# Performance work log

Measured on AMD Instinct MI355X. Metric: run time of the kernel, lower is better.

## Reference

```python
import jax, jax.numpy as jnp
import numpy as np

# RON cell constants (from repo defaults)
DT = 0.01
GAMMA = 1.0
EPS = 1.0
RHO_M = 1.0

T, N_INP = 2048, 128
N_MOD, N_HID = 64, 256


def setup_inputs() -> dict:
    key = jax.random.key(0)
    k = jax.random.split(key, 7)
    x = jax.random.normal(k[0], (T, N_INP), dtype=jnp.float32)
    initial_states = jax.random.normal(k[1], (N_MOD, 2, N_HID), dtype=jnp.float32)
    # wm: Linear(n_hid, n_hid, bias=False), rescaled to spectral radius rho_m
    wm = jax.random.normal(k[2], (N_HID, N_HID), dtype=jnp.float32) / np.float32(np.sqrt(N_HID))
    spec = np.abs(np.linalg.eigvals(np.asarray(wm, dtype=np.float64))).max()
    wm_weight = (wm * np.float32(RHO_M / spec)).astype(jnp.float32)
    # binary connection matrix (stored as float Parameter in the original)
    connection_matrix = (jax.random.uniform(k[3], (N_MOD, N_MOD)) < 0.5).astype(jnp.float32)
    x2h = jax.random.normal(k[4], (N_MOD, N_HID, N_INP), dtype=jnp.float32) / np.float32(np.sqrt(N_INP))
    h2h = jax.random.normal(k[5], (N_MOD, N_HID, N_HID), dtype=jnp.float32) / np.float32(np.sqrt(N_HID))
    bias = 0.1 * jax.random.normal(k[6], (N_MOD, N_HID), dtype=jnp.float32)
    return {
        "x": x,
        "initial_states": initial_states,
        "wm_weight": wm_weight,
        "connection_matrix": connection_matrix,
        "x2h": x2h,
        "h2h": h2h,
        "bias": bias,
    }


def reference(x, initial_states, wm_weight, connection_matrix, x2h, h2h, bias):
    """Returns (states_seq, feedback_seq).
    states_seq:   (T+1, n_modules, 2, n_hid)  -- state_list stacked
    feedback_seq: (T,   n_modules, n_hid)     -- per-step feedback (input_list minus the x[0] prefix)
    """

    def step(carry, x_t):
        states, outs = carry                       # (N,2,H), (N,H)
        # feedback = connection_matrix @ wm(prev_outs)
        fb = connection_matrix @ (outs @ wm_weight.T)            # (N, H)
        hy, hz = states[:, 0], states[:, 1]                       # (N, H)
        pre = (
            jnp.einsum("nhi,i->nh", x2h, x_t)
            + jnp.einsum("nho,no->nh", h2h, hy)
            + bias
            + fb
        )
        hz_new = hz + DT * (jnp.tanh(pre) - GAMMA * hy - EPS * hz)
        hy_new = hy + DT * hz_new
        new_states = jnp.stack([hy_new, hz_new], axis=1)          # (N, 2, H)
        # outs for next step = first state (hy), as in `outs = states[:, 0]`
        return (new_states, hy_new), (new_states, fb)

    outs0 = jnp.zeros((N_MOD, N_HID), dtype=x.dtype)  # initial_outs=None path
    (_, _), (states_hist, fb_hist) = jax.lax.scan(step, (initial_states, outs0), x)
    states_seq = jnp.concatenate([initial_states[None], states_hist], axis=0)
    return states_seq, fb_hist
```

## Files before the change

### kernel.cpp

```cpp
#include <hip/hip_runtime.h>
#include <hip/hip_bf16.h>
#include <math.h>

#define T_STEPS 2048
#define N_MOD   64
#define N_HID   256
#define N_INP   128

typedef unsigned long long ull;

__device__ __forceinline__ void AG_STF(float* p, float v) {
  __hip_atomic_store(p, v, __ATOMIC_RELAXED, __HIP_MEMORY_SCOPE_AGENT);
}
__device__ __forceinline__ void AG_STU(unsigned* p, unsigned v) {
  __hip_atomic_store(p, v, __ATOMIC_RELAXED, __HIP_MEMORY_SCOPE_AGENT);
}
__device__ __forceinline__ unsigned AG_LDU(const unsigned* p) {
  return __hip_atomic_load(p, __ATOMIC_RELAXED, __HIP_MEMORY_SCOPE_AGENT);
}

__global__ __launch_bounds__(512) void init_kernel(
    const float* __restrict__ init, float* __restrict__ out_states)
{
  const int idx = blockIdx.x * 512 + threadIdx.x;
  out_states[idx] = init[idx];
}

__global__ __launch_bounds__(256, 2) void xpre_kernel(
    const float* __restrict__ x, const float* __restrict__ x2h,
    float* __restrict__ out)
{
  __shared__ float xl[64 * N_INP];
  const int tb = blockIdx.x;
  const int n  = blockIdx.y;
  const int t  = threadIdx.x;

  const float4* xs  = (const float4*)(x + (size_t)tb * 64 * N_INP);
  float4*       xld = (float4*)xl;
  for (int k = t; k < 64 * N_INP / 4; k += 256) xld[k] = xs[k];

  float w[N_INP];
  const float* wrow = x2h + ((size_t)n * N_HID + t) * N_INP;
#pragma unroll
  for (int j = 0; j < N_INP; j += 4) {
    const float4 a = *(const float4*)(wrow + j);
    w[j] = a.x; w[j+1] = a.y; w[j+2] = a.z; w[j+3] = a.w;
  }
  __syncthreads();

  for (int tt = 0; tt < 64; ++tt) {
    float a0=0.f, a1=0.f, a2=0.f, a3=0.f;
#pragma unroll
    for (int j = 0; j < N_INP; j += 4) {
      const float4 h4 = *(const float4*)&xl[tt * N_INP + j];
      a0 = fmaf(w[j],   h4.x, a0);
      a1 = fmaf(w[j+1], h4.y, a1);
      a2 = fmaf(w[j+2], h4.z, a2);
      a3 = fmaf(w[j+3], h4.w, a3);
    }
    out[((size_t)(tb*64 + tt) * N_MOD + n) * N_HID + t] = (a0+a1)+(a2+a3);
  }
}

__global__ __launch_bounds__(256) void step_kernel(
    int k, const float* __restrict__ wm, const float* __restrict__ conn,
    const float* __restrict__ h2h, const float* __restrict__ bias,
    float* __restrict__ out_states, float* __restrict__ out_fb)
{
  const int b  = blockIdx.x;
  const int m  = b >> 2;
  const int q  = b & 3;
  const int i  = threadIdx.x;
  const int ro = i & 63;
  const int jq = i >> 6;

  __shared__ float hym[N_HID];
  __shared__ float u[N_HID];
  __shared__ float redr[256];
  __shared__ float redf[256];

  const float* hyk = out_states + (size_t)k * N_MOD * 512;

  hym[i] = hyk[(size_t)m * 512 + i];
  {
    float ua=0.f, ub=0.f, uc=0.f, ud=0.f;
#pragma unroll
    for (int mm = 0; mm < N_MOD; mm += 4) {
      ua = fmaf(conn[m * N_MOD + mm + 0], hyk[(size_t)(mm + 0) * 512 + i], ua);
      ub = fmaf(conn[m * N_MOD + mm + 1], hyk[(size_t)(mm + 1) * 512 + i], ub);
      uc = fmaf(conn[m * N_MOD + mm + 2], hyk[(size_t)(mm + 2) * 512 + i], uc);
      ud = fmaf(conn[m * N_MOD + mm + 3], hyk[(size_t)(mm + 3) * 512 + i], ud);
    }
    u[i] = (ua + ub) + (uc + ud);
  }
  float xq = 0.f, hyv = 0.f, hzv = 0.f, bv = 0.f;
  if (i < 64) {
    const int hu = q * 64 + i;
    xq  = out_fb[((size_t)k * N_MOD + m) * N_HID + hu];
    hyv = hyk[(size_t)m * 512 + hu];
    hzv = hyk[(size_t)m * 512 + 256 + hu];
    bv  = bias[m * N_HID + hu];
  }
  __syncthreads();

  {
    const int h = q * 64 + ro;
    const float* hrow = h2h + ((size_t)m * N_HID + h) * N_HID + jq * 64;
    const float* wrow = wm  + (size_t)h * N_HID + jq * 64;
    float r0=0.f, r1=0.f, r2=0.f, r3=0.f;
    float f0=0.f, f1=0.f, f2=0.f, f3=0.f;
#pragma unroll
    for (int j = 0; j < 64; j += 4) {
      const float4 a  = *(const float4*)(hrow + j);
      const float4 w4 = *(const float4*)(wrow + j);
      const float4 hv = *(const float4*)(&hym[jq * 64 + j]);
      const float4 uv = *(const float4*)(&u[jq * 64 + j]);
      r0 = fmaf(a.x, hv.x, r0);  f0 = fmaf(w4.x, uv.x, f0);
      r1 = fmaf(a.y, hv.y, r1);  f1 = fmaf(w4.y, uv.y, f1);
      r2 = fmaf(a.z, hv.z, r2);  f2 = fmaf(w4.z, uv.z, f2);
      r3 = fmaf(a.w, hv.w, r3);  f3 = fmaf(w4.w, uv.w, f3);
    }
    redr[i] = (r0 + r1) + (r2 + r3);
    redf[i] = (f0 + f1) + (f2 + f3);
  }
  __syncthreads();

  if (i < 64) {
    const int hu = q * 64 + i;
    const float r  = (redr[i] + redr[i + 64]) + (redr[i + 128] + redr[i + 192]);
    const float fb = (k == 0) ? 0.f
                   : (redf[i] + redf[i + 64]) + (redf[i + 128] + redf[i + 192]);
    const float pre = xq + r + bv + fb;
    const float th  = tanhf(pre);
    const float hzn = hzv + 0.01f * (th - hyv - hzv);
    const float hyn = hyv + 0.01f * hzn;
    const size_t ob = ((size_t)(k + 1) * N_MOD + m) * 512;
    out_states[ob + hu]       = hyn;
    out_states[ob + 256 + hu] = hzn;
    out_fb[((size_t)k * N_MOD + m) * N_HID + hu] = fb;
  }
}

__global__ __launch_bounds__(256) void archnet_persist(
    const float* __restrict__ init, const float* __restrict__ wm,
    const float* __restrict__ conn, const float* __restrict__ h2h,
    const float* __restrict__ bias,
    float* __restrict__ out_states, float* __restrict__ out_fb,
    unsigned* __restrict__ flags)
{
  __shared__ float wA[64 * 256];
  __shared__ float hym_l[4 * 68];
  __shared__ float u_l[4 * 68];
  __shared__ float connrow[N_MOD];

  const int b  = blockIdx.x;
  const int m  = b >> 2;
  const int q  = b & 3;
  const int i  = threadIdx.x;
  const int r  = i >> 2;
  const int c4 = i & 3;
  const int hq = q * 64 + r;
  const int pi = (i >> 6) * 68 + (i & 63);

  if (i < N_MOD) connrow[i] = conn[m * N_MOD + i];
  u_l[pi] = 0.f;

  for (int idx = i; idx < 64 * 64; idx += 256) {
    const int rr = idx >> 6, g = idx & 63;
    const float4 a = *(const float4*)(h2h + ((size_t)m * N_HID + q * 64 + rr) * N_HID + g * 4);
    *(float4*)&wA[rr * 256 + (g ^ (rr & 7)) * 4] = a;
  }

  float hyv = 0.f, hzv = 0.f, bv = 0.f, xq = 0.f;
  if (c4 == 0) {
    hyv = init[(size_t)m * 512 + hq];
    hzv = init[(size_t)m * 512 + 256 + hq];
    bv  = bias[m * N_HID + hq];
    xq  = out_fb[(size_t)m * N_HID + hq];
  }

  const float* wrow = wm + (size_t)hq * N_HID + c4 * 64;

  for (int k = 0; k < T_STEPS; ++k) {
    if (k > 0 && i < 64) {
      const unsigned kk = (unsigned)k;
      for (;;) {
        const unsigned f0 = AG_LDU(&flags[i * 4 + 0]);
        const unsigned f1 = AG_LDU(&flags[i * 4 + 1]);
        const unsigned f2 = AG_LDU(&flags[i * 4 + 2]);
        const unsigned f3 = AG_LDU(&flags[i * 4 + 3]);
        if (!__any(f0 < kk || f1 < kk || f2 < kk || f3 < kk)) break;
        __builtin_amdgcn_s_sleep(1);
      }
    }
    __syncthreads();

    const float* hyk = out_states + (size_t)k * (N_MOD * 512);
    hym_l[pi] = hyk[(size_t)m * 512 + i];
    if (k > 0) {
      float ua=0.f, ub=0.f, uc=0.f, ud=0.f;
#pragma unroll
      for (int mm = 0; mm < N_MOD; mm += 4) {
        ua = fmaf(connrow[mm+0], hyk[(size_t)(mm+0) * 512 + i], ua);
        ub = fmaf(connrow[mm+1], hyk[(size_t)(mm+1) * 512 + i], ub);
        uc = fmaf(connrow[mm+2], hyk[(size_t)(mm+2) * 512 + i], uc);
        ud = fmaf(connrow[mm+3], hyk[(size_t)(mm+3) * 512 + i], ud);
      }
      u_l[pi] = (ua + ub) + (uc + ud);
    }
    __syncthreads();

    float rsum, fsum;
    {
      float r0=0.f, r1=0.f, r2=0.f, r3=0.f;
      float f0=0.f, f1=0.f, f2=0.f, f3=0.f;
#pragma unroll
      for (int j = 0; j < 16; ++j) {
        const int gs = ((c4 * 16 + j) ^ (r & 7)) * 4;
        const float4 a  = *(const float4*)&wA[r * 256 + gs];
        const float4 w4 = *(const float4*)(wrow + j * 4);
        const float4 hv = *(const float4*)&hym_l[c4 * 68 + j * 4];
        const float4 uv = *(const float4*)&u_l[c4 * 68 + j * 4];
        r0 = fmaf(a.x, hv.x, r0);  f0 = fmaf(w4.x, uv.x, f0);
        r1 = fmaf(a.y, hv.y, r1);  f1 = fmaf(w4.y, uv.y, f1);
        r2 = fmaf(a.z, hv.z, r2);  f2 = fmaf(w4.z, uv.z, f2);
        r3 = fmaf(a.w, hv.w, r3);  f3 = fmaf(w4.w, uv.w, f3);
      }
      rsum = (r0 + r1) + (r2 + r3);
      fsum = (f0 + f1) + (f2 + f3);
      rsum += __shfl_xor(rsum, 1); rsum += __shfl_xor(rsum, 2);
      fsum += __shfl_xor(fsum, 1); fsum += __shfl_xor(fsum, 2);
    }

    float fbv = 0.f;
    if (c4 == 0) {
      fbv = (k == 0) ? 0.f : fsum;
      const float pre = xq + rsum + bv + fbv;
      const float th  = tanhf(pre);
      hzv = hzv + 0.01f * (th - hyv - hzv);
      hyv = hyv + 0.01f * hzv;
      AG_STF(out_states + (size_t)(k + 1) * (N_MOD * 512) + (size_t)m * 512 + hq,
             hyv);
    }
    __syncthreads();
    if (i == 0) AG_STU(&flags[b], (unsigned)(k + 1));

    if (c4 == 0) {
      const size_t ob = ((size_t)(k + 1) * N_MOD + m) * 512;
      out_states[ob + 256 + hq] = hzv;
      out_fb[((size_t)k * N_MOD + m) * N_HID + hq] = fbv;
      if (k + 1 < T_STEPS)
        xq = out_fb[((size_t)(k + 1) * N_MOD + m) * N_HID + hq];
    }
  }
}

extern "C" void kernel_launch(void* const* d_in, const int* in_sizes, int n_in,
                              void* d_out, int out_size, void* d_ws, size_t ws_size,
                              hipStream_t stream) {
  const float* x    = (const float*)d_in[0];
  const float* init = (const float*)d_in[1];
  const float* wmw  = (const float*)d_in[2];
  const float* conn = (const float*)d_in[3];
  const float* x2h  = (const float*)d_in[4];
  const float* h2h  = (const float*)d_in[5];
  const float* bias = (const float*)d_in[6];

  float* out_states = (float*)d_out;
  float* out_fb     = out_states + (size_t)(T_STEPS+1) * N_MOD * 2 * N_HID;

  unsigned* flags = (unsigned*)d_ws;
  hipMemsetAsync(d_ws, 0, 1024, stream);

  init_kernel<<<64, 512, 0, stream>>>(init, out_states);
  xpre_kernel<<<dim3(T_STEPS/64, N_MOD), dim3(256), 0, stream>>>(x, x2h, out_fb);

  void* args[] = {
    (void*)&init, (void*)&wmw, (void*)&conn, (void*)&h2h, (void*)&bias,
    (void*)&out_states, (void*)&out_fb, (void*)&flags
  };
  hipError_t err = hipLaunchCooperativeKernel((void*)archnet_persist,
                                              dim3(256), dim3(256),
                                              args, 0, stream);
  if (err != hipSuccess) {
    for (int k = 0; k < T_STEPS; ++k)
      step_kernel<<<256, 256, 0, stream>>>(k, wmw, conn, h2h, bias,
                                           out_states, out_fb);
  }
}
```

Before: 10.42 ms.

## Restructure persistent recurrence loop to shorten per-step critical path between blocks

```diff
diff --git a/kernel.cpp b/kernel.cpp
--- a/kernel.cpp
+++ b/kernel.cpp
@@ -6,8 +6,6 @@
 #define N_MOD   64
 #define N_HID   256
 #define N_INP   128
-
-typedef unsigned long long ull;
 
 __device__ __forceinline__ void AG_STF(float* p, float v) {
   __hip_atomic_store(p, v, __ATOMIC_RELAXED, __HIP_MEMORY_SCOPE_AGENT);
@@ -151,19 +149,22 @@
   __shared__ float wA[64 * 256];
   __shared__ float hym_l[4 * 68];
   __shared__ float u_l[4 * 68];
+  __shared__ float redr[256];
+  __shared__ float redf[256];
   __shared__ float connrow[N_MOD];
 
   const int b  = blockIdx.x;
   const int m  = b >> 2;
   const int q  = b & 3;
   const int i  = threadIdx.x;
-  const int r  = i >> 2;
-  const int c4 = i & 3;
-  const int hq = q * 64 + r;
-  const int pi = (i >> 6) * 68 + (i & 63);
+  const int ro = i & 63;
+  const int jq = i >> 6;
+  const int hu = q * 64 + ro;
+  const int pi = jq * 68 + ro;
 
   if (i < N_MOD) connrow[i] = conn[m * N_MOD + i];
   u_l[pi] = 0.f;
+  hym_l[pi] = init[(size_t)m * 512 + i];
 
   for (int idx = i; idx < 64 * 64; idx += 256) {
     const int rr = idx >> 6, g = idx & 63;
@@ -172,85 +173,109 @@
   }
 
   float hyv = 0.f, hzv = 0.f, bv = 0.f, xq = 0.f;
-  if (c4 == 0) {
-    hyv = init[(size_t)m * 512 + hq];
-    hzv = init[(size_t)m * 512 + 256 + hq];
-    bv  = bias[m * N_HID + hq];
-    xq  = out_fb[(size_t)m * N_HID + hq];
-  }
-
-  const float* wrow = wm + (size_t)hq * N_HID + c4 * 64;
+  if (i < 64) {
+    hyv = init[(size_t)m * 512 + hu];
+    hzv = init[(size_t)m * 512 + 256 + hu];
+    bv  = bias[m * N_HID + hu];
+    xq  = out_fb[(size_t)m * N_HID + hu];
+  }
+  __syncthreads();
+
+  {
+    const float* wrow = wm + (size_t)hu * N_HID + jq * 64;
+    float r0=0.f, r1=0.f, r2=0.f, r3=0.f;
+    float f0=0.f, f1=0.f, f2=0.f, f3=0.f;
+#pragma unroll
+    for (int j = 0; j < 16; ++j) {
+      const int gs = ((jq * 16 + j) ^ (ro & 7)) * 4;
+      const float4 a  = *(const float4*)&wA[ro * 256 + gs];
+      const float4 w4 = *(const float4*)(wrow + j * 4);
+      const float4 hv = *(const float4*)&hym_l[jq * 68 + j * 4];
+      const float4 uv = *(const float4*)&u_l[jq * 68 + j * 4];
+      r0 = fmaf(a.x, hv.x, r0);  f0 = fmaf(w4.x, uv.x, f0);
+      r1 = fmaf(a.y, hv.y, r1);  f1 = fmaf(w4.y, uv.y, f1);
+      r2 = fmaf(a.z, hv.z, r2);  f2 = fmaf(w4.z, uv.z, f2);
+      r3 = fmaf(a.w, hv.w, r3);  f3 = fmaf(w4.w, uv.w, f3);
+    }
+    redr[i] = (r0 + r1) + (r2 + r3);
+    redf[i] = (f0 + f1) + (f2 + f3);
+  }
+  __syncthreads();
 
   for (int k = 0; k < T_STEPS; ++k) {
-    if (k > 0 && i < 64) {
-      const unsigned kk = (unsigned)k;
+    if (i < 64) {
+      const float r  = (redr[i] + redr[i + 64]) + (redr[i + 128] + redr[i + 192]);
+      const float fb = (redf[i] + redf[i + 64]) + (redf[i + 128] + redf[i + 192]);
+      const float pre = xq + r + bv + fb;
+      const float th  = tanhf(pre);
+      hzv = hzv + 0.01f * (th - hyv - hzv);
+      hyv = hyv + 0.01f * hzv;
+
+      AG_STF(out_states + (size_t)(k + 1) * (N_MOD * 512) + (size_t)m * 512 + hu,
+             hyv);
+      asm volatile("s_waitcnt vmcnt(0)" ::: "memory");
+      if (i == 0) AG_STU(&flags[b], (unsigned)(k + 1));
+
+      const size_t ob = ((size_t)(k + 1) * N_MOD + m) * 512;
+      out_states[ob + 256 + hu] = hzv;
+      out_fb[((size_t)k * N_MOD + m) * N_HID + hu] = fb;
+      if (k + 1 < T_STEPS)
+        xq = out_fb[((size_t)(k + 1) * N_MOD + m) * N_HID + hu];
+    } else if (i < 128 && k + 1 < T_STEPS) {
+      const unsigned kk = (unsigned)(k + 1);
+      const int fb4 = (i - 64) * 4;
       for (;;) {
-        const unsigned f0 = AG_LDU(&flags[i * 4 + 0]);
-        const unsigned f1 = AG_LDU(&flags[i * 4 + 1]);
-        const unsigned f2 = AG_LDU(&flags[i * 4 + 2]);
-        const unsigned f3 = AG_LDU(&flags[i * 4 + 3]);
+        const unsigned f0 = AG_LDU(&flags[fb4 + 0]);
+        const unsigned f1 = AG_LDU(&flags[fb4 + 1]);
+        const unsigned f2 = AG_LDU(&flags[fb4 + 2]);
+        const unsigned f3 = AG_LDU(&flags[fb4 + 3]);
         if (!__any(f0 < kk || f1 < kk || f2 < kk || f3 < kk)) break;
         __builtin_amdgcn_s_sleep(1);
       }
     }
     __syncthreads();
 
-    const float* hyk = out_states + (size_t)k * (N_MOD * 512);
-    hym_l[pi] = hyk[(size_t)m * 512 + i];
-    if (k > 0) {
-      float ua=0.f, ub=0.f, uc=0.f, ud=0.f;
-#pragma unroll
-      for (int mm = 0; mm < N_MOD; mm += 4) {
-        ua = fmaf(connrow[mm+0], hyk[(size_t)(mm+0) * 512 + i], ua);
-        ub = fmaf(connrow[mm+1], hyk[(size_t)(mm+1) * 512 + i], ub);
-        uc = fmaf(connrow[mm+2], hyk[(size_t)(mm+2) * 512 + i], uc);
-        ud = fmaf(connrow[mm+3], hyk[(size_t)(mm+3) * 512 + i], ud);
+    if (k + 1 < T_STEPS) {
+      float4 wreg[16];
+      {
+        const float* wrow = wm + (size_t)hu * N_HID + jq * 64;
+#pragma unroll
+        for (int j = 0; j < 16; ++j) wreg[j] = ((const float4*)wrow)[j];
       }
-      u_l[pi] = (ua + ub) + (uc + ud);
-    }
-    __syncthreads();
-
-    float rsum, fsum;
-    {
-      float r0=0.f, r1=0.f, r2=0.f, r3=0.f;
-      float f0=0.f, f1=0.f, f2=0.f, f3=0.f;
-#pragma unroll
-      for (int j = 0; j < 16; ++j) {
-        const int gs = ((c4 * 16 + j) ^ (r & 7)) * 4;
-        const float4 a  = *(const float4*)&wA[r * 256 + gs];
-        const float4 w4 = *(const float4*)(wrow + j * 4);
-        const float4 hv = *(const float4*)&hym_l[c4 * 68 + j * 4];
-        const float4 uv = *(const float4*)&u_l[c4 * 68 + j * 4];
-        r0 = fmaf(a.x, hv.x, r0);  f0 = fmaf(w4.x, uv.x, f0);
-        r1 = fmaf(a.y, hv.y, r1);  f1 = fmaf(w4.y, uv.y, f1);
-        r2 = fmaf(a.z, hv.z, r2);  f2 = fmaf(w4.z, uv.z, f2);
-        r3 = fmaf(a.w, hv.w, r3);  f3 = fmaf(w4.w, uv.w, f3);
+
+      const float* hyk1 = out_states + (size_t)(k + 1) * (N_MOD * 512);
+      hym_l[pi] = hyk1[(size_t)m * 512 + i];
+      {
+        float ua=0.f, ub=0.f, uc=0.f, ud=0.f;
+#pragma unroll
+        for (int mm = 0; mm < N_MOD; mm += 4) {
+          ua = fmaf(connrow[mm+0], hyk1[(size_t)(mm+0) * 512 + i], ua);
+          ub = fmaf(connrow[mm+1], hyk1[(size_t)(mm+1) * 512 + i], ub);
+          uc = fmaf(connrow[mm+2], hyk1[(size_t)(mm+2) * 512 + i], uc);
+          ud = fmaf(connrow[mm+3], hyk1[(size_t)(mm+3) * 512 + i], ud);
+        }
+        u_l[pi] = (ua + ub) + (uc + ud);
       }
-      rsum = (r0 + r1) + (r2 + r3);
-      fsum = (f0 + f1) + (f2 + f3);
-      rsum += __shfl_xor(rsum, 1); rsum += __shfl_xor(rsum, 2);
-      fsum += __shfl_xor(fsum, 1); fsum += __shfl_xor(fsum, 2);
-    }
-
-    float fbv = 0.f;
-    if (c4 == 0) {
-      fbv = (k == 0) ? 0.f : fsum;
-      const float pre = xq + rsum + bv + fbv;
-      const float th  = tanhf(pre);
-      hzv = hzv + 0.01f * (th - hyv - hzv);
-      hyv = hyv + 0.01f * hzv;
-      AG_STF(out_states + (size_t)(k + 1) * (N_MOD * 512) + (size_t)m * 512 + hq,
-             hyv);
-    }
-    __syncthreads();
-    if (i == 0) AG_STU(&flags[b], (unsigned)(k + 1));
-
-    if (c4 == 0) {
-      const size_t ob = ((size_t)(k + 1) * N_MOD + m) * 512;
-      out_states[ob + 256 + hq] = hzv;
-      out_fb[((size_t)k * N_MOD + m) * N_HID + hq] = fbv;
-      if (k + 1 < T_STEPS)
-        xq = out_fb[((size_t)(k + 1) * N_MOD + m) * N_HID + hq];
+      __syncthreads();
+
+      {
+        float r0=0.f, r1=0.f, r2=0.f, r3=0.f;
+        float f0=0.f, f1=0.f, f2=0.f, f3=0.f;
+#pragma unroll
+        for (int j = 0; j < 16; ++j) {
+          const int gs = ((jq * 16 + j) ^ (ro & 7)) * 4;
+          const float4 a  = *(const float4*)&wA[ro * 256 + gs];
+          const float4 hv = *(const float4*)&hym_l[jq * 68 + j * 4];
+          const float4 uv = *(const float4*)&u_l[jq * 68 + j * 4];
+          r0 = fmaf(a.x, hv.x, r0);  f0 = fmaf(wreg[j].x, uv.x, f0);
+          r1 = fmaf(a.y, hv.y, r1);  f1 = fmaf(wreg[j].y, uv.y, f1);
+          r2 = fmaf(a.z, hv.z, r2);  f2 = fmaf(wreg[j].z, uv.z, f2);
+          r3 = fmaf(a.w, hv.w, r3);  f3 = fmaf(wreg[j].w, uv.w, f3);
+        }
+        redr[i] = (r0 + r1) + (r2 + r3);
+        redf[i] = (f0 + f1) + (f2 + f3);
+      }
+      __syncthreads();
     }
   }
 }
```

After: 17.43 ms. +67.3%, slower.
